# Optimization experiments

Measured on AMD Instinct MI355X. Metric: run time of the kernel, lower is better.

The kernel has to match this reference:

```python
import jax, jax.numpy as jnp
import numpy as np

N = 50000      # nodes
E = 800000     # edges (avg degree 16)
D_IN = 16      # raw node feature dim
D = 64         # d_model
H = 8          # heads
DH = D // H    # dim_head = 8
L = 2          # num_encoder_layers
EPS = 1e-5
SCALE = float(np.sqrt(DH))


def _xavier(key, shape):
    fan_in, fan_out = shape[-2], shape[-1]
    a = float(np.sqrt(6.0 / (fan_in + fan_out)))
    return jax.random.uniform(key, shape, jnp.float32, -a, a)


def setup_inputs() -> dict:
    key = jax.random.key(0)
    ks = jax.random.split(key, 20)
    feat = jax.random.normal(ks[0], (N, D_IN), jnp.float32)
    src = jax.random.randint(ks[1], (E,), 0, N, jnp.int32)
    dst = jax.random.randint(ks[2], (E,), 0, N, jnp.int32)
    return {
        "feat": feat,
        "src": src,
        "dst": dst,
        "W_emb": _xavier(ks[3], (D_IN, D)),
        "b_emb": jnp.zeros((D,), jnp.float32),
        "Wq": _xavier(ks[4], (L, D, D)),
        "Wk": _xavier(ks[5], (L, D, D)),
        "Wv": _xavier(ks[6], (L, D, D)),
        "Wo": _xavier(ks[7], (L, D, D)),
        "bo": jnp.zeros((L, D), jnp.float32),
        "bn1_g": jnp.ones((L, D), jnp.float32),
        "bn1_b": jnp.zeros((L, D), jnp.float32),
        "W1": _xavier(ks[8], (L, D, 2 * D)),
        "b1": jnp.zeros((L, 2 * D), jnp.float32),
        "W2": _xavier(ks[9], (L, 2 * D, D)),
        "b2": jnp.zeros((L, D), jnp.float32),
        "bn2_g": jnp.ones((L, D), jnp.float32),
        "bn2_b": jnp.zeros((L, D), jnp.float32),
    }


def _batch_norm(x, g, b):
    # BatchNorm1d (training-mode forward: batch statistics, biased var)
    mu = jnp.mean(x, axis=0)
    var = jnp.var(x, axis=0)
    return (x - mu) / jnp.sqrt(var + EPS) * g + b


def _layer(h, src, dst, Wq, Wk, Wv, Wo, bo, bn1_g, bn1_b, W1, b1, W2, b2, bn2_g, bn2_b):
    h_in1 = h
    Q = (h @ Wq).reshape(N, H, DH)
    K = (h @ Wk).reshape(N, H, DH)
    V = (h @ Wv).reshape(N, H, DH)
    # SDDMM: per-edge dot(K[src], Q[dst]) -> [E, H]
    e = jnp.sum(K[src] * Q[dst], axis=-1)
    # scaled_exp: exp(clamp(score/sqrt(dh), -10, 10)) stored as edge 'score'
    e = jnp.exp(jnp.clip(e / SCALE, -10.0, 10.0))
    # reduce_func then applies a softmax over mailbox scores (double exp, faithful)
    m = jax.ops.segment_max(e, dst, num_segments=N)          # [N, H]
    w = jnp.exp(e - m[dst])                                   # [E, H]
    s = jax.ops.segment_sum(w, dst, num_segments=N)           # [N, H]
    alpha = w / s[dst]                                        # [E, H]
    out = jax.ops.segment_sum(alpha[:, :, None] * V[src], dst, num_segments=N)
    h = out.reshape(N, D) @ Wo + bo
    h = _batch_norm(h_in1 + h, bn1_g, bn1_b)
    h_in2 = h
    h = jax.nn.relu(h @ W1 + b1) @ W2 + b2
    h = _batch_norm(h + h_in2, bn2_g, bn2_b)
    return h


def reference(feat, src, dst, W_emb, b_emb, Wq, Wk, Wv, Wo, bo, bn1_g, bn1_b,
              W1, b1, W2, b2, bn2_g, bn2_b):
    h = feat @ W_emb + b_emb  # embedding_h (dropout=0)
    for l in range(L):
        h = _layer(h, src, dst, Wq[l], Wk[l], Wv[l], Wo[l], bo[l],
                   bn1_g[l], bn1_b[l], W1[l], b1[l], W2[l], b2[l],
                   bn2_g[l], bn2_b[l])
    return h
```

## Files before the change

kernel.cpp:

```cpp
#include <hip/hip_runtime.h>

#define NNODES 50000
#define NEDGES 800000
#define DM 64
#define NH 8
#define DH 8
#define EPSN 1e-5f
#define INV_SCALE 0.3535533905932738f
#define SCAN_BLOCKS 200
#define SCAN_CHUNK  250

template<int KA, int KB, int R, bool RELU, bool RES, bool STATS, bool BNRES>
__global__ __launch_bounds__(256, 2) void gemm_k(const float* __restrict__ A,
    const float* __restrict__ W, int woff,
    const float* __restrict__ bias, int boff,
    float* __restrict__ C, float* __restrict__ stats,
    const float* __restrict__ bnstats, const float* __restrict__ bng, int bgoff,
    const float* __restrict__ bnb, int bboff, int Nrows)
{
    constexpr int CG   = KB / 4;
    constexpr int RG   = 256 / CG;
    constexpr int ROWS = RG * R;
    constexpr int APAD = KA + 4;
    constexpr int KAq  = KA / 4;

    __shared__ __align__(16) float sW[KA * KB];
    __shared__ __align__(16) float sA[ROWS * APAD];

    const int tid  = threadIdx.x;
    const int row0 = blockIdx.x * ROWS;

    for (int i4 = tid; i4 < KA * KB / 4; i4 += 256)
        *(float4*)&sW[i4 * 4] = ((const float4*)(W + woff))[i4];
    for (int i4 = tid; i4 < ROWS * KAq; i4 += 256) {
        int r = i4 / KAq, kq = i4 - r * KAq;
        int gr = row0 + r;
        float4 v = make_float4(0.f, 0.f, 0.f, 0.f);
        if (gr < Nrows) v = ((const float4*)A)[(size_t)gr * KAq + kq];
        *(float4*)&sA[r * APAD + kq * 4] = v;
    }
    __syncthreads();

    const int cg = tid % CG, rg = tid / CG;
    const int c0 = cg * 4, r0 = rg * R;

    float4 acc[R];
#pragma unroll
    for (int rr = 0; rr < R; rr++) acc[rr] = make_float4(0.f, 0.f, 0.f, 0.f);

#pragma unroll 2
    for (int k = 0; k < KA; k += 4) {
        float4 w0 = *(const float4*)&sW[(k + 0) * KB + c0];
        float4 w1 = *(const float4*)&sW[(k + 1) * KB + c0];
        float4 w2 = *(const float4*)&sW[(k + 2) * KB + c0];
        float4 w3 = *(const float4*)&sW[(k + 3) * KB + c0];
#pragma unroll
        for (int rr = 0; rr < R; rr++) {
            float4 av = *(const float4*)&sA[(r0 + rr) * APAD + k];
            acc[rr].x += av.x * w0.x + av.y * w1.x + av.z * w2.x + av.w * w3.x;
            acc[rr].y += av.x * w0.y + av.y * w1.y + av.z * w2.y + av.w * w3.y;
            acc[rr].z += av.x * w0.z + av.y * w1.z + av.z * w2.z + av.w * w3.z;
            acc[rr].w += av.x * w0.w + av.y * w1.w + av.z * w2.w + av.w * w3.w;
        }
    }

    float4 bv = make_float4(0.f, 0.f, 0.f, 0.f);
    if (bias) {
        bv.x = bias[boff + c0];     bv.y = bias[boff + c0 + 1];
        bv.z = bias[boff + c0 + 2]; bv.w = bias[boff + c0 + 3];
    }

    float4 scR = make_float4(1.f, 1.f, 1.f, 1.f);
    float4 ofR = make_float4(0.f, 0.f, 0.f, 0.f);
    if (BNRES) {
        const float inv_n = 1.0f / NNODES;
#pragma unroll
        for (int j = 0; j < 4; j++) {
            float mu   = bnstats[c0 + j] * inv_n;
            float var  = bnstats[KB + c0 + j] * inv_n - mu * mu;
            float istd = rsqrtf(fmaxf(var, 0.f) + EPSN);
            float s    = istd * bng[bgoff + c0 + j];
            ((float*)&scR)[j] = s;
            ((float*)&ofR)[j] = bnb[bboff + c0 + j] - mu * s;
        }
    }

    float4 vals[R];
#pragma unroll
    for (int rr = 0; rr < R; rr++) {
        int grow = row0 + r0 + rr;
        bool valid = grow < Nrows;
        float4 v;
        v.x = acc[rr].x + bv.x; v.y = acc[rr].y + bv.y;
        v.z = acc[rr].z + bv.z; v.w = acc[rr].w + bv.w;
        if (RELU) {
            v.x = fmaxf(v.x, 0.f); v.y = fmaxf(v.y, 0.f);
            v.z = fmaxf(v.z, 0.f); v.w = fmaxf(v.w, 0.f);
        }
        if (valid) {
            if (RES) {
                float4 old = *(const float4*)&C[(size_t)grow * KB + c0];
                if (BNRES) {
                    old.x = old.x * scR.x + ofR.x;
                    old.y = old.y * scR.y + ofR.y;
                    old.z = old.z * scR.z + ofR.z;
                    old.w = old.w * scR.w + ofR.w;
                }
                v.x += old.x; v.y += old.y; v.z += old.z; v.w += old.w;
            }
            *(float4*)&C[(size_t)grow * KB + c0] = v;
        } else {
            v = make_float4(0.f, 0.f, 0.f, 0.f);
        }
        vals[rr] = v;
    }

    if (STATS) {
        __syncthreads();
        float4 cs = make_float4(0.f, 0.f, 0.f, 0.f);
#pragma unroll
        for (int rr = 0; rr < R; rr++) {
            cs.x += vals[rr].x; cs.y += vals[rr].y;
            cs.z += vals[rr].z; cs.w += vals[rr].w;
        }
        *(float4*)&sA[rg * KB + c0] = cs;
        __syncthreads();
        if (tid < KB) {
            float s = 0.f;
#pragma unroll
            for (int g = 0; g < RG; g++) s += sA[g * KB + tid];
            atomicAdd(&stats[tid], s);
        }
        __syncthreads();
        float4 cq = make_float4(0.f, 0.f, 0.f, 0.f);
#pragma unroll
        for (int rr = 0; rr < R; rr++) {
            cq.x += vals[rr].x * vals[rr].x; cq.y += vals[rr].y * vals[rr].y;
            cq.z += vals[rr].z * vals[rr].z; cq.w += vals[rr].w * vals[rr].w;
        }
        *(float4*)&sA[rg * KB + c0] = cq;
        __syncthreads();
        if (tid < KB) {
            float s = 0.f;
#pragma unroll
            for (int g = 0; g < RG; g++) s += sA[g * KB + tid];
            atomicAdd(&stats[KB + tid], s);
        }
    }
}

template<bool BNIN>
__global__ __launch_bounds__(256, 2) void qkv_k(const float* __restrict__ A,
    const float* __restrict__ Wq, const float* __restrict__ Wk,
    const float* __restrict__ Wv, int woff,
    float* __restrict__ Qo, float* __restrict__ Ko, float* __restrict__ Vo,
    const float* __restrict__ bnstats, const float* __restrict__ bng, int bgoff,
    const float* __restrict__ bnb, int bboff, int Nrows)
{
    constexpr int APAD = 68;
    __shared__ __align__(16) float sW[64 * 64];
    __shared__ __align__(16) float sA[64 * APAD];

    const int tid  = threadIdx.x;
    const int row0 = blockIdx.x * 64;

    {
        const int kq = tid & 15, cc = kq * 4;
        float4 sc = make_float4(1.f, 1.f, 1.f, 1.f);
        float4 of = make_float4(0.f, 0.f, 0.f, 0.f);
        if (BNIN) {
            const float inv_n = 1.0f / NNODES;
#pragma unroll
            for (int j = 0; j < 4; j++) {
                float mu   = bnstats[cc + j] * inv_n;
                float var  = bnstats[64 + cc + j] * inv_n - mu * mu;
                float istd = rsqrtf(fmaxf(var, 0.f) + EPSN);
                float s    = istd * bng[bgoff + cc + j];
                ((float*)&sc)[j] = s;
                ((float*)&of)[j] = bnb[bboff + cc + j] - mu * s;
            }
        }
        for (int i4 = tid; i4 < 64 * 16; i4 += 256) {
            int r = i4 >> 4;
            int gr = row0 + r;
            float4 v = make_float4(0.f, 0.f, 0.f, 0.f);
            if (gr < Nrows) {
                v = ((const float4*)A)[(size_t)gr * 16 + kq];
                if (BNIN) {
                    v.x = v.x * sc.x + of.x; v.y = v.y * sc.y + of.y;
                    v.z = v.z * sc.z + of.z; v.w = v.w * sc.w + of.w;
                }
            }
            *(float4*)&sA[r * APAD + cc] = v;
        }
    }

    const float* Ws[3]   = {Wq, Wk, Wv};
    float*       Outs[3] = {Qo, Ko, Vo};

    const int cg = tid & 15, rg = tid >> 4;
    const int c0 = cg * 4, r0 = rg * 4;

    for (int m = 0; m < 3; m++) {
        __syncthreads();
        for (int i4 = tid; i4 < 1024; i4 += 256)
            *(float4*)&sW[i4 * 4] = ((const float4*)(Ws[m] + woff))[i4];
        __syncthreads();

        float4 acc[4];
#pragma unroll
        for (int rr = 0; rr < 4; rr++) acc[rr] = make_float4(0.f, 0.f, 0.f, 0.f);

#pragma unroll 2
        for (int k = 0; k < 64; k += 4) {
            float4 w0 = *(const float4*)&sW[(k + 0) * 64 + c0];
            float4 w1 = *(const float4*)&sW[(k + 1) * 64 + c0];
            float4 w2 = *(const float4*)&sW[(k + 2) * 64 + c0];
            float4 w3 = *(const float4*)&sW[(k + 3) * 64 + c0];
#pragma unroll
            for (int rr = 0; rr < 4; rr++) {
                float4 av = *(const float4*)&sA[(r0 + rr) * APAD + k];
                acc[rr].x += av.x * w0.x + av.y * w1.x + av.z * w2.x + av.w * w3.x;
                acc[rr].y += av.x * w0.y + av.y * w1.y + av.z * w2.y + av.w * w3.y;
                acc[rr].z += av.x * w0.z + av.y * w1.z + av.z * w2.z + av.w * w3.z;
                acc[rr].w += av.x * w0.w + av.y * w1.w + av.z * w2.w + av.w * w3.w;
            }
        }

#pragma unroll
        for (int rr = 0; rr < 4; rr++) {
            int grow = row0 + r0 + rr;
            if (grow < Nrows)
                *(float4*)&Outs[m][(size_t)grow * 64 + c0] = acc[rr];
        }
    }
}

__global__ __launch_bounds__(256, 4) void ffn_k(float* __restrict__ H,
    const float* __restrict__ W1, int w1off,
    const float* __restrict__ b1, int b1off,
    const float* __restrict__ W2, int w2off,
    const float* __restrict__ b2, int b2off,
    const float* __restrict__ bnstats,
    const float* __restrict__ bng, int bgoff,
    const float* __restrict__ bnb, int bboff,
    float* __restrict__ stats2, int Nrows)
{
    constexpr int APAD = 68, FPAD = 132;
    __shared__ __align__(16) float sA[32 * APAD];
    __shared__ __align__(16) float sF[32 * FPAD];

    const int tid  = threadIdx.x;
    const int row0 = blockIdx.x * 32;

    const float4* __restrict__ W1g = (const float4*)(W1 + w1off);
    const float4* __restrict__ W2g = (const float4*)(W2 + w2off);

    {
        const int kq = tid & 15, cc = kq * 4;
        const float inv_n = 1.0f / NNODES;
        float4 sc, of;
#pragma unroll
        for (int j = 0; j < 4; j++) {
            float mu   = bnstats[cc + j] * inv_n;
            float var  = bnstats[64 + cc + j] * inv_n - mu * mu;
            float istd = rsqrtf(fmaxf(var, 0.f) + EPSN);
            float s    = istd * bng[bgoff + cc + j];
            ((float*)&sc)[j] = s;
            ((float*)&of)[j] = bnb[bboff + cc + j] - mu * s;
        }
        for (int i4 = tid; i4 < 512; i4 += 256) {
            int r = i4 >> 4;
            int gr = row0 + r;
            float4 v = make_float4(0.f, 0.f, 0.f, 0.f);
            if (gr < Nrows) {
                v = ((const float4*)H)[(size_t)gr * 16 + kq];
                v.x = v.x * sc.x + of.x; v.y = v.y * sc.y + of.y;
                v.z = v.z * sc.z + of.z; v.w = v.w * sc.w + of.w;
            }
            *(float4*)&sA[r * APAD + cc] = v;
        }
    }
    __syncthreads();

    {
        const int cg = tid & 31, rg = tid >> 5;
        const int c0 = cg * 4, r0 = rg * 4;
        float4 acc[4];
#pragma unroll
        for (int rr = 0; rr < 4; rr++) acc[rr] = make_float4(0.f, 0.f, 0.f, 0.f);
#pragma unroll 2
        for (int k = 0; k < 64; k += 4) {
            float4 w0 = W1g[(k + 0) * 32 + cg];
            float4 w1 = W1g[(k + 1) * 32 + cg];
            float4 w2 = W1g[(k + 2) * 32 + cg];
            float4 w3 = W1g[(k + 3) * 32 + cg];
#pragma unroll
            for (int rr = 0; rr < 4; rr++) {
                float4 av = *(const float4*)&sA[(r0 + rr) * APAD + k];
                acc[rr].x += av.x * w0.x + av.y * w1.x + av.z * w2.x + av.w * w3.x;
                acc[rr].y += av.x * w0.y + av.y * w1.y + av.z * w2.y + av.w * w3.y;
                acc[rr].z += av.x * w0.z + av.y * w1.z + av.z * w2.z + av.w * w3.z;
                acc[rr].w += av.x * w0.w + av.y * w1.w + av.z * w2.w + av.w * w3.w;
            }
        }
        float4 bb;
        bb.x = b1[b1off + c0];     bb.y = b1[b1off + c0 + 1];
        bb.z = b1[b1off + c0 + 2]; bb.w = b1[b1off + c0 + 3];
#pragma unroll
        for (int rr = 0; rr < 4; rr++) {
            float4 v;
            v.x = fmaxf(acc[rr].x + bb.x, 0.f);
            v.y = fmaxf(acc[rr].y + bb.y, 0.f);
            v.z = fmaxf(acc[rr].z + bb.z, 0.f);
            v.w = fmaxf(acc[rr].w + bb.w, 0.f);
            *(float4*)&sF[(r0 + rr) * FPAD + c0] = v;
        }
    }
    __syncthreads();

    const int cg = tid & 15, rg = tid >> 4;
    const int c0 = cg * 4, r0 = rg * 2;
    float4 acc[2];
#pragma unroll
    for (int rr = 0; rr < 2; rr++) acc[rr] = make_float4(0.f, 0.f, 0.f, 0.f);
#pragma unroll 2
    for (int k = 0; k < 128; k += 4) {
        float4 w0 = W2g[(k + 0) * 16 + cg];
        float4 w1 = W2g[(k + 1) * 16 + cg];
        float4 w2 = W2g[(k + 2) * 16 + cg];
        float4 w3 = W2g[(k + 3) * 16 + cg];
#pragma unroll
        for (int rr = 0; rr < 2; rr++) {
            float4 fv = *(const float4*)&sF[(r0 + rr) * FPAD + k];
            acc[rr].x += fv.x * w0.x + fv.y * w1.x + fv.z * w2.x + fv.w * w3.x;
            acc[rr].y += fv.x * w0.y + fv.y * w1.y + fv.z * w2.y + fv.w * w3.y;
            acc[rr].z += fv.x * w0.z + fv.y * w1.z + fv.z * w2.z + fv.w * w3.z;
            acc[rr].w += fv.x * w0.w + fv.y * w1.w + fv.z * w2.w + fv.w * w3.w;
        }
    }
    float4 bb;
    bb.x = b2[b2off + c0];     bb.y = b2[b2off + c0 + 1];
    bb.z = b2[b2off + c0 + 2]; bb.w = b2[b2off + c0 + 3];

    float4 vals[2];
#pragma unroll
    for (int rr = 0; rr < 2; rr++) {
        int grow = row0 + r0 + rr;
        bool valid = grow < Nrows;
        float4 res = *(const float4*)&sA[(r0 + rr) * APAD + c0];
        float4 v;
        v.x = acc[rr].x + bb.x + res.x;
        v.y = acc[rr].y + bb.y + res.y;
        v.z = acc[rr].z + bb.z + res.z;
        v.w = acc[rr].w + bb.w + res.w;
        if (valid) {
            *(float4*)&H[(size_t)grow * 64 + c0] = v;
        } else {
            v = make_float4(0.f, 0.f, 0.f, 0.f);
        }
        vals[rr] = v;
    }

    __syncthreads();
    float4 cs;
    cs.x = vals[0].x + vals[1].x; cs.y = vals[0].y + vals[1].y;
    cs.z = vals[0].z + vals[1].z; cs.w = vals[0].w + vals[1].w;
    *(float4*)&sA[rg * 64 + c0] = cs;
    __syncthreads();
    if (tid < 64) {
        float s = 0.f;
#pragma unroll
        for (int g = 0; g < 16; g++) s += sA[g * 64 + tid];
        atomicAdd(&stats2[tid], s);
    }
    __syncthreads();
    float4 cq;
    cq.x = vals[0].x * vals[0].x + vals[1].x * vals[1].x;
    cq.y = vals[0].y * vals[0].y + vals[1].y * vals[1].y;
    cq.z = vals[0].z * vals[0].z + vals[1].z * vals[1].z;
    cq.w = vals[0].w * vals[0].w + vals[1].w * vals[1].w;
    *(float4*)&sA[rg * 64 + c0] = cq;
    __syncthreads();
    if (tid < 64) {
        float s = 0.f;
#pragma unroll
        for (int g = 0; g < 16; g++) s += sA[g * 64 + tid];
        atomicAdd(&stats2[64 + tid], s);
    }
}

__global__ __launch_bounds__(256) void bn_apply(const float* __restrict__ Hin,
    float* __restrict__ Hout, const float* __restrict__ stats,
    const float* __restrict__ g, int goff, const float* __restrict__ b, int boff)
{
    int i = blockIdx.x * 256 + threadIdx.x;
    if (i >= NNODES * DM) return;
    int c = i & 63;
    float mu  = stats[c] * (1.0f / NNODES);
    float var = stats[64 + c] * (1.0f / NNODES) - mu * mu;
    float istd = rsqrtf(fmaxf(var, 0.0f) + EPSN);
    Hout[i] = (Hin[i] - mu) * istd * g[goff + c] + b[boff + c];
}

__global__ __launch_bounds__(256) void zero_int_k(int* __restrict__ p, int n)
{
    int i = blockIdx.x * 256 + threadIdx.x;
    if (i < n) p[i] = 0;
}

__global__ __launch_bounds__(256) void count_k(const int* __restrict__ dst,
                                               int* __restrict__ cursor)
{
    int e = blockIdx.x * 256 + threadIdx.x;
    if (e < NEDGES) atomicAdd(&cursor[dst[e]], 1);
}

__global__ __launch_bounds__(256) void csr_scanA(const int* __restrict__ cursor,
                                                 int* __restrict__ bsum)
{
    __shared__ int red[256];
    const int base = blockIdx.x * SCAN_CHUNK;
    int s = 0;
    for (int i = threadIdx.x; i < SCAN_CHUNK; i += 256) s += cursor[base + i];
    red[threadIdx.x] = s;
    __syncthreads();
    for (int o = 128; o > 0; o >>= 1) {
        if (threadIdx.x < o) red[threadIdx.x] += red[threadIdx.x + o];
        __syncthreads();
    }
    if (threadIdx.x == 0) bsum[blockIdx.x] = red[0];
}

__global__ __launch_bounds__(256) void csr_scanB(int* __restrict__ bsum)
{
    __shared__ int t[256];
    const int tid = threadIdx.x;
    int v = (tid < SCAN_BLOCKS) ? bsum[tid] : 0;
    t[tid] = v;
    __syncthreads();
    for (int off = 1; off < 256; off <<= 1) {
        int x = (tid >= off) ? t[tid - off] : 0;
        __syncthreads();
        t[tid] += x;
        __syncthreads();
    }
    if (tid < SCAN_BLOCKS) bsum[tid] = t[tid] - v;
}

__global__ __launch_bounds__(256) void csr_scanC(int* __restrict__ cursor,
    int* __restrict__ rowptr, const int* __restrict__ bsum)
{
    __shared__ int t[256];
    const int base = blockIdx.x * SCAN_CHUNK;
    const int tid  = threadIdx.x;
    int deg = (tid < SCAN_CHUNK) ? cursor[base + tid] : 0;
    t[tid] = deg;
    __syncthreads();
    for (int off = 1; off < 256; off <<= 1) {
        int x = (tid >= off) ? t[tid - off] : 0;
        __syncthreads();
        t[tid] += x;
        __syncthreads();
    }
    int excl = bsum[blockIdx.x] + t[tid] - deg;
    if (tid < SCAN_CHUNK) {
        rowptr[base + tid] = excl;
        cursor[base + tid] = excl;
    }
    if (blockIdx.x == 0 && tid == 0) rowptr[NNODES] = NEDGES;
}

__global__ __launch_bounds__(256) void fill_k(const int* __restrict__ src,
    const int* __restrict__ dst, int* __restrict__ cursor,
    int* __restrict__ nbr)
{
    int e = blockIdx.x * 256 + threadIdx.x;
    if (e >= NEDGES) return;
    int pos = atomicAdd(&cursor[dst[e]], 1);
    nbr[pos] = src[e];
}

__global__ __launch_bounds__(256) void attn_fused_k(const float* __restrict__ Q,
    const float* __restrict__ K, const float* __restrict__ V,
    const int* __restrict__ rowptr, const int* __restrict__ nbr,
    float* __restrict__ U)
{
    const int w = threadIdx.x >> 6;
    const int d = blockIdx.x * 4 + w;
    if (d >= NNODES) return;
    const int l  = threadIdx.x & 63;
    const int el = l >> 3;
    const int h  = l & 7;
    const int e0 = rowptr[d], e1 = rowptr[d + 1];
    const int deg = e1 - e0;

    if (deg == 0) {
        U[(size_t)d * DM + h * DH + el] = 0.f;
        return;
    }

    const float4* qp = (const float4*)(Q + (size_t)d * DM + h * DH);
    const float4 q0 = qp[0], q1 = qp[1];

    float m = 0.0f;
    float S = 0.0f;
    float u[8] = {0.f, 0.f, 0.f, 0.f, 0.f, 0.f, 0.f, 0.f};

    for (int base = 0; base < deg; base += 16) {
        const int i0 = base + el, i1 = base + 8 + el;
        const bool v0ok = i0 < deg, v1ok = i1 < deg;
        const int s0 = nbr[e0 + (v0ok ? i0 : 0)];
        const int s1 = nbr[e0 + (v1ok ? i1 : 0)];

        const float4* kp0 = (const float4*)(K + (size_t)s0 * DM + h * DH);
        const float4* vp0 = (const float4*)(V + (size_t)s0 * DM + h * DH);
        const float4* kp1 = (const float4*)(K + (size_t)s1 * DM + h * DH);
        const float4* vp1 = (const float4*)(V + (size_t)s1 * DM + h * DH);
        float4 ka0 = kp0[0], ka1 = kp0[1];
        float4 kb0 = kp1[0], kb1 = kp1[1];
        float4 va0 = vp0[0], va1 = vp0[1];
        float4 vb0 = vp1[0], vb1 = vp1[1];

        float d0 = ka0.x * q0.x + ka0.y * q0.y + ka0.z * q0.z + ka0.w * q0.w
                 + ka1.x * q1.x + ka1.y * q1.y + ka1.z * q1.z + ka1.w * q1.w;
        float d1 = kb0.x * q0.x + kb0.y * q0.y + kb0.z * q0.z + kb0.w * q0.w
                 + kb1.x * q1.x + kb1.y * q1.y + kb1.z * q1.z + kb1.w * q1.w;

        float ev0 = __expf(fminf(fmaxf(d0 * INV_SCALE, -10.f), 10.f));
        float ev1 = __expf(fminf(fmaxf(d1 * INV_SCALE, -10.f), 10.f));
        if (!v0ok) ev0 = 0.f;
        if (!v1ok) ev1 = 0.f;

        float bm = fmaxf(ev0, ev1);
        bm = fmaxf(bm, __shfl_xor(bm, 8, 64));
        bm = fmaxf(bm, __shfl_xor(bm, 16, 64));
        bm = fmaxf(bm, __shfl_xor(bm, 32, 64));

        const float mn = fmaxf(m, bm);
        const float r  = __expf(m - mn);
        const float w0 = v0ok ? __expf(ev0 - mn) : 0.f;
        const float w1 = v1ok ? __expf(ev1 - mn) : 0.f;

        S = S * r + w0 + w1;
        u[0] = u[0] * r + w0 * va0.x + w1 * vb0.x;
        u[1] = u[1] * r + w0 * va0.y + w1 * vb0.y;
        u[2] = u[2] * r + w0 * va0.z + w1 * vb0.z;
        u[3] = u[3] * r + w0 * va0.w + w1 * vb0.w;
        u[4] = u[4] * r + w0 * va1.x + w1 * vb1.x;
        u[5] = u[5] * r + w0 * va1.y + w1 * vb1.y;
        u[6] = u[6] * r + w0 * va1.z + w1 * vb1.z;
        u[7] = u[7] * r + w0 * va1.w + w1 * vb1.w;
        m = mn;
    }

#pragma unroll
    for (int off = 8; off <= 32; off <<= 1) {
        S += __shfl_xor(S, off, 64);
#pragma unroll
        for (int j = 0; j < 8; j++) u[j] += __shfl_xor(u[j], off, 64);
    }

    const float out = (S > 0.f) ? u[el] / S : 0.f;
    U[(size_t)d * DM + h * DH + el] = out;
}

__global__ __launch_bounds__(256) void fill_const_k(float* __restrict__ out, int n)
{
    int i = blockIdx.x * 256 + threadIdx.x;
    if (i < n) out[i] = 100.0f;
}

extern "C" void kernel_launch(void* const* d_in, const int* in_sizes, int n_in,
                              void* d_out, int out_size, void* d_ws, size_t ws_size,
                              hipStream_t stream)
{
    const int expect[18] = {800000, 800000, 800000, 1024, 64,
                            8192, 8192, 8192, 8192, 128,
                            128, 128, 16384, 256, 16384, 128, 128, 128};
    bool order_ok = (n_in == 18) && (out_size == NNODES * DM);
    if (order_ok)
        for (int i = 0; i < 18; i++)
            if (in_sizes[i] != expect[i]) { order_ok = false; break; }
    if (!order_ok) {
        fill_const_k<<<(out_size + 255) / 256, 256, 0, stream>>>((float*)d_out,
                                                                 out_size);
        return;
    }

    const float* feat  = (const float*)d_in[0];
    const int*   src   = (const int*)d_in[1];
    const int*   dst   = (const int*)d_in[2];
    const float* W_emb = (const float*)d_in[3];
    const float* b_emb = (const float*)d_in[4];
    const float* Wq    = (const float*)d_in[5];
    const float* Wk    = (const float*)d_in[6];
    const float* Wv    = (const float*)d_in[7];
    const float* Wo    = (const float*)d_in[8];
    const float* bo    = (const float*)d_in[9];
    const float* bn1_g = (const float*)d_in[10];
    const float* bn1_b = (const float*)d_in[11];
    const float* W1    = (const float*)d_in[12];
    const float* b1    = (const float*)d_in[13];
    const float* W2    = (const float*)d_in[14];
    const float* b2    = (const float*)d_in[15];
    const float* bn2_g = (const float*)d_in[16];
    const float* bn2_b = (const float*)d_in[17];

    const size_t ND = (size_t)NNODES * DM;
    float* ws     = (float*)d_ws;
    float* Hb     = ws;
    float* Qb     = Hb + ND;
    float* Kb     = Qb + ND;
    float* Vb     = Kb + ND;
    float* Ub     = Vb + ND;
    float* stats  = Ub + ND;
    int*   rowptr = (int*)(stats + 256);
    int*   cursor = rowptr + (NNODES + 1);
    int*   bsum   = cursor + NNODES;
    int*   nbr    = bsum + SCAN_BLOCKS;

    float* statsA = stats;
    float* statsB = stats + 128;

    const size_t BASE = (5 * ND + 256) * 4
                      + ((NNODES + 1) + NNODES + SCAN_BLOCKS + NEDGES) * 4;
    if (ws_size < BASE) {
        fill_const_k<<<(out_size + 255) / 256, 256, 0, stream>>>((float*)d_out,
                                                                 out_size);
        return;
    }

    const int g64 = (NNODES + 63) / 64;
    const int g32 = (NNODES + 31) / 32;
    const int gND = (int)(ND / 256);
    const int gE  = (NEDGES + 255) / 256;
    const int gAT = (NNODES + 3) / 4;

    zero_int_k<<<(NNODES + 255) / 256, 256, 0, stream>>>(cursor, NNODES);
    count_k<<<gE, 256, 0, stream>>>(dst, cursor);
    csr_scanA<<<SCAN_BLOCKS, 256, 0, stream>>>(cursor, bsum);
    csr_scanB<<<1, 256, 0, stream>>>(bsum);
    csr_scanC<<<SCAN_BLOCKS, 256, 0, stream>>>(cursor, rowptr, bsum);
    fill_k<<<gE, 256, 0, stream>>>(src, dst, cursor, nbr);

    gemm_k<16, 64, 4, false, false, false, false>
        <<<g64, 256, 0, stream>>>(feat, W_emb, 0, b_emb, 0, Hb, nullptr,
                                  nullptr, nullptr, 0, nullptr, 0, NNODES);

    for (int l = 0; l < 2; l++) {
        const int woff  = l * DM * DM;
        const int w1off = l * DM * 2 * DM;
        const int boff  = l * DM;
        const int b1off = l * 2 * DM;
        const int poff  = (l - 1) * DM;

        if (l == 0)
            qkv_k<false><<<g64, 256, 0, stream>>>(Hb, Wq, Wk, Wv, woff,
                Qb, Kb, Vb, nullptr, nullptr, 0, nullptr, 0, NNODES);
        else
            qkv_k<true><<<g64, 256, 0, stream>>>(Hb, Wq, Wk, Wv, woff,
                Qb, Kb, Vb, statsB, bn2_g, poff, bn2_b, poff, NNODES);

        attn_fused_k<<<gAT, 256, 0, stream>>>(Qb, Kb, Vb, rowptr, nbr, Ub);

        hipMemsetAsync(statsA, 0, 128 * 4, stream);
        if (l == 0)
            gemm_k<64, 64, 4, false, true, true, false>
                <<<g64, 256, 0, stream>>>(Ub, Wo, woff, bo, boff, Hb, statsA,
                                          nullptr, nullptr, 0, nullptr, 0, NNODES);
        else
            gemm_k<64, 64, 4, false, true, true, true>
                <<<g64, 256, 0, stream>>>(Ub, Wo, woff, bo, boff, Hb, statsA,
                                          statsB, bn2_g, poff, bn2_b, poff, NNODES);

        hipMemsetAsync(statsB, 0, 128 * 4, stream);
        ffn_k<<<g32, 256, 0, stream>>>(Hb, W1, w1off, b1, b1off,
                                       W2, w1off, b2, boff,
                                       statsA, bn1_g, boff, bn1_b, boff,
                                       statsB, NNODES);
    }

    bn_apply<<<gND, 256, 0, stream>>>(Hb, (float*)d_out, statsB,
                                      bn2_g, DM, bn2_b, DM);
}
```

Baseline: 557.4 us.

## Restructure FFN kernel so each wavefront owns eight rows without block syncs

The fused FFN kernel now gives each 64-thread wavefront its own 8-row slice, with private LDS buffers for the input and hidden activations. The two block-wide barriers between the load, first GEMM and second GEMM stages are removed. Each lane computes one output column (two for the hidden layer) across 8 rows, reading A values as LDS broadcasts and weights as coalesced scalar loads. The per-column BN statistics reduction shrinks from 16 partials to 4. In exchange, each lane does scalar weight loads per k instead of float4 loads, which means more load instructions per FMA.

```diff
diff --git a/kernel.cpp b/kernel.cpp
--- a/kernel.cpp
+++ b/kernel.cpp
@@ -246,147 +246,125 @@
     const float* __restrict__ bnb, int bboff,
     float* __restrict__ stats2, int Nrows)
 {
-    constexpr int APAD = 68, FPAD = 132;
-    __shared__ __align__(16) float sA[32 * APAD];
-    __shared__ __align__(16) float sF[32 * FPAD];
+    constexpr int APAD = 68;
+    __shared__ __align__(16) float sA[4][8 * APAD];
+    __shared__ __align__(16) float sF[4][8 * 128];
+    __shared__ __align__(16) float sR[4 * 64];
 
     const int tid  = threadIdx.x;
-    const int row0 = blockIdx.x * 32;
-
-    const float4* __restrict__ W1g = (const float4*)(W1 + w1off);
-    const float4* __restrict__ W2g = (const float4*)(W2 + w2off);
+    const int w    = tid >> 6;
+    const int c    = tid & 63;
+    const int row0 = blockIdx.x * 32 + w * 8;
+
+    float* sAw = sA[w];
+    float* sFw = sF[w];
+    const float* __restrict__ W1g = W1 + w1off;
+    const float* __restrict__ W2g = W2 + w2off;
 
     {
-        const int kq = tid & 15, cc = kq * 4;
+        const int q = c & 15;
+        const int r = c >> 4;
         const float inv_n = 1.0f / NNODES;
         float4 sc, of;
 #pragma unroll
         for (int j = 0; j < 4; j++) {
-            float mu   = bnstats[cc + j] * inv_n;
-            float var  = bnstats[64 + cc + j] * inv_n - mu * mu;
+            float mu   = bnstats[q * 4 + j] * inv_n;
+            float var  = bnstats[64 + q * 4 + j] * inv_n - mu * mu;
             float istd = rsqrtf(fmaxf(var, 0.f) + EPSN);
-            float s    = istd * bng[bgoff + cc + j];
+            float s    = istd * bng[bgoff + q * 4 + j];
             ((float*)&sc)[j] = s;
-            ((float*)&of)[j] = bnb[bboff + cc + j] - mu * s;
-        }
-        for (int i4 = tid; i4 < 512; i4 += 256) {
-            int r = i4 >> 4;
-            int gr = row0 + r;
+            ((float*)&of)[j] = bnb[bboff + q * 4 + j] - mu * s;
+        }
+#pragma unroll
+        for (int rr = 0; rr < 2; rr++) {
+            int lr = r + rr * 4;
+            int gr = row0 + lr;
             float4 v = make_float4(0.f, 0.f, 0.f, 0.f);
             if (gr < Nrows) {
-                v = ((const float4*)H)[(size_t)gr * 16 + kq];
+                v = ((const float4*)H)[(size_t)gr * 16 + q];
                 v.x = v.x * sc.x + of.x; v.y = v.y * sc.y + of.y;
                 v.z = v.z * sc.z + of.z; v.w = v.w * sc.w + of.w;
             }
-            *(float4*)&sA[r * APAD + cc] = v;
-        }
-    }
-    __syncthreads();
+            *(float4*)&sAw[lr * APAD + q * 4] = v;
+        }
+    }
 
     {
-        const int cg = tid & 31, rg = tid >> 5;
-        const int c0 = cg * 4, r0 = rg * 4;
-        float4 acc[4];
-#pragma unroll
-        for (int rr = 0; rr < 4; rr++) acc[rr] = make_float4(0.f, 0.f, 0.f, 0.f);
+        float accL[8], accH[8];
+#pragma unroll
+        for (int r = 0; r < 8; r++) { accL[r] = 0.f; accH[r] = 0.f; }
 #pragma unroll 2
-        for (int k = 0; k < 64; k += 4) {
-            float4 w0 = W1g[(k + 0) * 32 + cg];
-            float4 w1 = W1g[(k + 1) * 32 + cg];
-            float4 w2 = W1g[(k + 2) * 32 + cg];
-            float4 w3 = W1g[(k + 3) * 32 + cg];
-#pragma unroll
-            for (int rr = 0; rr < 4; rr++) {
-                float4 av = *(const float4*)&sA[(r0 + rr) * APAD + k];
-                acc[rr].x += av.x * w0.x + av.y * w1.x + av.z * w2.x + av.w * w3.x;
-                acc[rr].y += av.x * w0.y + av.y * w1.y + av.z * w2.y + av.w * w3.y;
-                acc[rr].z += av.x * w0.z + av.y * w1.z + av.z * w2.z + av.w * w3.z;
-                acc[rr].w += av.x * w0.w + av.y * w1.w + av.z * w2.w + av.w * w3.w;
+        for (int k4 = 0; k4 < 16; k4++) {
+            float4 av[8];
+#pragma unroll
+            for (int r = 0; r < 8; r++)
+                av[r] = *(const float4*)&sAw[r * APAD + k4 * 4];
+#pragma unroll
+            for (int j = 0; j < 4; j++) {
+                int k = k4 * 4 + j;
+                float wl = W1g[k * 128 + c];
+                float wh = W1g[k * 128 + c + 64];
+#pragma unroll
+                for (int r = 0; r < 8; r++) {
+                    float a = ((const float*)&av[r])[j];
+                    accL[r] += a * wl;
+                    accH[r] += a * wh;
+                }
             }
         }
-        float4 bb;
-        bb.x = b1[b1off + c0];     bb.y = b1[b1off + c0 + 1];
-        bb.z = b1[b1off + c0 + 2]; bb.w = b1[b1off + c0 + 3];
-#pragma unroll
-        for (int rr = 0; rr < 4; rr++) {
-            float4 v;
-            v.x = fmaxf(acc[rr].x + bb.x, 0.f);
-            v.y = fmaxf(acc[rr].y + bb.y, 0.f);
-            v.z = fmaxf(acc[rr].z + bb.z, 0.f);
-            v.w = fmaxf(acc[rr].w + bb.w, 0.f);
-            *(float4*)&sF[(r0 + rr) * FPAD + c0] = v;
-        }
-    }
-    __syncthreads();
-
-    const int cg = tid & 15, rg = tid >> 4;
-    const int c0 = cg * 4, r0 = rg * 2;
-    float4 acc[2];
-#pragma unroll
-    for (int rr = 0; rr < 2; rr++) acc[rr] = make_float4(0.f, 0.f, 0.f, 0.f);
+        float bL = b1[b1off + c], bH = b1[b1off + c + 64];
+#pragma unroll
+        for (int r = 0; r < 8; r++) {
+            sFw[r * 128 + c]      = fmaxf(accL[r] + bL, 0.f);
+            sFw[r * 128 + c + 64] = fmaxf(accH[r] + bH, 0.f);
+        }
+    }
+
+    float acc2[8];
+#pragma unroll
+    for (int r = 0; r < 8; r++) acc2[r] = 0.f;
 #pragma unroll 2
-    for (int k = 0; k < 128; k += 4) {
-        float4 w0 = W2g[(k + 0) * 16 + cg];
-        float4 w1 = W2g[(k + 1) * 16 + cg];
-        float4 w2 = W2g[(k + 2) * 16 + cg];
-        float4 w3 = W2g[(k + 3) * 16 + cg];
-#pragma unroll
-        for (int rr = 0; rr < 2; rr++) {
-            float4 fv = *(const float4*)&sF[(r0 + rr) * FPAD + k];
-            acc[rr].x += fv.x * w0.x + fv.y * w1.x + fv.z * w2.x + fv.w * w3.x;
-            acc[rr].y += fv.x * w0.y + fv.y * w1.y + fv.z * w2.y + fv.w * w3.y;
-            acc[rr].z += fv.x * w0.z + fv.y * w1.z + fv.z * w2.z + fv.w * w3.z;
-            acc[rr].w += fv.x * w0.w + fv.y * w1.w + fv.z * w2.w + fv.w * w3.w;
-        }
-    }
-    float4 bb;
-    bb.x = b2[b2off + c0];     bb.y = b2[b2off + c0 + 1];
-    bb.z = b2[b2off + c0 + 2]; bb.w = b2[b2off + c0 + 3];
-
-    float4 vals[2];
-#pragma unroll
-    for (int rr = 0; rr < 2; rr++) {
-        int grow = row0 + r0 + rr;
-        bool valid = grow < Nrows;
-        float4 res = *(const float4*)&sA[(r0 + rr) * APAD + c0];
-        float4 v;
-        v.x = acc[rr].x + bb.x + res.x;
-        v.y = acc[rr].y + bb.y + res.y;
-        v.z = acc[rr].z + bb.z + res.z;
-        v.w = acc[rr].w + bb.w + res.w;
-        if (valid) {
-            *(float4*)&H[(size_t)grow * 64 + c0] = v;
-        } else {
-            v = make_float4(0.f, 0.f, 0.f, 0.f);
-        }
-        vals[rr] = v;
-    }
-
-    __syncthreads();
-    float4 cs;
-    cs.x = vals[0].x + vals[1].x; cs.y = vals[0].y + vals[1].y;
-    cs.z = vals[0].z + vals[1].z; cs.w = vals[0].w + vals[1].w;
-    *(float4*)&sA[rg * 64 + c0] = cs;
+    for (int k4 = 0; k4 < 32; k4++) {
+        float4 fv[8];
+#pragma unroll
+        for (int r = 0; r < 8; r++)
+            fv[r] = *(const float4*)&sFw[r * 128 + k4 * 4];
+#pragma unroll
+        for (int j = 0; j < 4; j++) {
+            int k = k4 * 4 + j;
+            float w2 = W2g[k * 64 + c];
+#pragma unroll
+            for (int r = 0; r < 8; r++)
+                acc2[r] += ((const float*)&fv[r])[j] * w2;
+        }
+    }
+
+    const float bc = b2[b2off + c];
+    float vals[8];
+#pragma unroll
+    for (int r = 0; r < 8; r++) {
+        int grow = row0 + r;
+        float v = acc2[r] + bc + sAw[r * APAD + c];
+        if (grow < Nrows) H[(size_t)grow * 64 + c] = v;
+        else v = 0.f;
+        vals[r] = v;
+    }
+
+    float s = 0.f, qsum = 0.f;
+#pragma unroll
+    for (int r = 0; r < 8; r++) { s += vals[r]; qsum += vals[r] * vals[r]; }
+    sR[w * 64 + c] = s;
     __syncthreads();
     if (tid < 64) {
-        float s = 0.f;
-#pragma unroll
-        for (int g = 0; g < 16; g++) s += sA[g * 64 + tid];
-        atomicAdd(&stats2[tid], s);
+        float t = sR[tid] + sR[64 + tid] + sR[128 + tid] + sR[192 + tid];
+        atomicAdd(&stats2[tid], t);
     }
     __syncthreads();
-    float4 cq;
-    cq.x = vals[0].x * vals[0].x + vals[1].x * vals[1].x;
-    cq.y = vals[0].y * vals[0].y + vals[1].y * vals[1].y;
-    cq.z = vals[0].z * vals[0].z + vals[1].z * vals[1].z;
-    cq.w = vals[0].w * vals[0].w + vals[1].w * vals[1].w;
-    *(float4*)&sA[rg * 64 + c0] = cq;
+    sR[w * 64 + c] = qsum;
     __syncthreads();
     if (tid < 64) {
-        float s = 0.f;
-#pragma unroll
-        for (int g = 0; g < 16; g++) s += sA[g * 64 + tid];
-        atomicAdd(&stats2[64 + tid], s);
+        float t = sR[tid] + sR[64 + tid] + sR[128 + tid] + sR[192 + tid];
+        atomicAdd(&stats2[64 + tid], t);
     }
 }
 
```

Measured after the change: 567.0 us. Within noise of the previous version (+1.7%).
